# Performance work log

Hardware: AMD Instinct MI355X
Metric: run time of the kernel (lower is better)

The kernel has to match this reference:

```python
import jax, jax.numpy as jnp
import numpy as np

EPS = 1e-12  # matches torch F.normalize default eps

def _l2_normalize(v, axis=-1):
    n = jnp.sqrt(jnp.sum(v * v, axis=axis, keepdims=True))
    return v / jnp.maximum(n, EPS)

def setup_inputs() -> dict:
    key = jax.random.key(0)
    k1, k2, k3 = jax.random.split(key, 3)
    B, S, D_IN, D_OUT, T = 4, 4096, 1024, 1024, 1024
    std = 1.0 / np.sqrt(D_IN)
    return {
        "x": jax.random.normal(k1, (B, S, D_IN), dtype=jnp.float32),
        "key_tokens": jax.random.normal(k2, (T, D_IN), dtype=jnp.float32) * std,
        "value_tokens": jax.random.normal(k3, (T, D_OUT), dtype=jnp.float32) * std,
        "temp": jnp.ones((T, 1), dtype=jnp.float32),
    }

def reference(x, key_tokens, value_tokens, temp):
    # x: [B,S,D_in]; key_tokens: [T,D_in]; value_tokens: [T,D_out]; temp: [T,1]
    x_norm = _l2_normalize(x)                      # [B,S,D_in]
    k_norm = _l2_normalize(key_tokens)             # [T,D_in]
    sim = jnp.einsum('bsd,td->bst', x_norm, k_norm)  # [B,S,T]
    sim = sim * jax.nn.sigmoid(temp).reshape(1, 1, -1)
    # mod_softmax: scale each row to RMS-norm sqrt(T), then exact GELU
    T = sim.shape[-1]
    scale = jnp.sqrt(jnp.float32(T)) / jnp.sqrt(jnp.sum(sim * sim, axis=-1, keepdims=True))
    weights = jax.nn.gelu(sim * scale, approximate=False)  # [B,S,T]
    return jnp.einsum('bst,to->bso', weights, value_tokens)  # [B,S,D_out]
```

## Files before the change

### kernel.cpp

```cpp
#include <hip/hip_runtime.h>
#include <math.h>

typedef __attribute__((ext_vector_type(8))) short short8;
typedef __attribute__((ext_vector_type(4))) float floatx4;

__device__ __forceinline__ float bf2f(unsigned short u) {
    union { unsigned int u; float f; } v;
    v.u = ((unsigned int)u) << 16;
    return v.f;
}

__device__ __forceinline__ unsigned short f2bf(float f) {
    union { float f; unsigned int u; } v;
    v.f = f;
    unsigned int r = v.u + 0x7fffu + ((v.u >> 16) & 1u);
    return (unsigned short)(r >> 16);
}

__device__ __forceinline__ void gload16_lds(const void* g, void* l) {
    __builtin_amdgcn_global_load_lds(
        (const __attribute__((address_space(1))) unsigned int*)g,
        (__attribute__((address_space(3))) unsigned int*)l, 16, 0, 0);
}

__device__ __forceinline__ ushort4 cvt4(float4 v, float fa) {
    ushort4 o;
    o.x = f2bf(v.x * fa); o.y = f2bf(v.y * fa);
    o.z = f2bf(v.z * fa); o.w = f2bf(v.w * fa);
    return o;
}

__global__ __launch_bounds__(256) void prep_kernel(
    const float* __restrict__ x, const float* __restrict__ key,
    const float* __restrict__ temp, const float* __restrict__ val,
    unsigned short* __restrict__ xb, unsigned short* __restrict__ kf,
    unsigned short* __restrict__ VT, float* __restrict__ rowsq,
    int M, int T, int D, int Dout, int nRowBlocks) {
    const int bid = blockIdx.x;
    if (bid < nRowBlocks) {
        const int lane = threadIdx.x & 63;
        const int nWaves = nRowBlocks << 2;
        const int totRows = M + T;
        for (int row = (bid << 2) | (int)(threadIdx.x >> 6); row < totRows;
             row += nWaves) {
            const bool isx = row < M;
            const int r = isx ? row : row - M;
            const float4* s4 =
                (const float4*)(isx ? (x + (size_t)r * D) : (key + (size_t)r * D));
            float4 v0 = s4[lane];
            float4 v1 = s4[lane + 64];
            float4 v2 = s4[lane + 128];
            float4 v3 = s4[lane + 192];
            float s = v0.x * v0.x + v0.y * v0.y + v0.z * v0.z + v0.w * v0.w;
            s += v1.x * v1.x + v1.y * v1.y + v1.z * v1.z + v1.w * v1.w;
            s += v2.x * v2.x + v2.y * v2.y + v2.z * v2.z + v2.w * v2.w;
            s += v3.x * v3.x + v3.y * v3.y + v3.z * v3.z + v3.w * v3.w;
#pragma unroll
            for (int o = 32; o > 0; o >>= 1) s += __shfl_xor(s, o, 64);
            float fa = 1.0f / fmaxf(sqrtf(s), 1e-12f);
            if (isx) {
                if (lane == 0) rowsq[r] = 0.0f;
            } else {
                fa = fa / (1.0f + expf(-temp[r]));
            }
            ushort4* dst =
                (ushort4*)(isx ? (xb + (size_t)r * D) : (kf + (size_t)r * D));
            dst[lane] = cvt4(v0, fa);
            dst[lane + 64] = cvt4(v1, fa);
            dst[lane + 128] = cvt4(v2, fa);
            dst[lane + 192] = cvt4(v3, fa);
        }
    } else {
        __shared__ unsigned short tile[64][65];
        const int idx = bid - nRowBlocks;
        const int nCt = Dout >> 6;
        const int c0 = (idx % nCt) * 64;
        const int r0 = (idx / nCt) * 64;
        const int t = threadIdx.x;
        for (int i = t; i < 4096; i += 256) {
            int rr = i >> 6, cc = i & 63;
            tile[rr][cc] = f2bf(val[(size_t)(r0 + rr) * Dout + c0 + cc]);
        }
        __syncthreads();
        for (int i = t; i < 4096; i += 256) {
            int rr = i >> 6, cc = i & 63;
            VT[(size_t)(c0 + rr) * T + r0 + cc] = tile[cc][rr];
        }
    }
}

template <int MODE>
__global__ __launch_bounds__(256, 2) void gemm_pipe(
    const unsigned short* __restrict__ A, const unsigned short* __restrict__ B,
    void* __restrict__ Cv, float* __restrict__ rowsq, int M, int N, int K) {
    __shared__ __align__(16) char smem[73728];
    const int tid = threadIdx.x;
    const int lane = tid & 63;
    const int w = tid >> 6;
    const int wr = w >> 1;
    const int wc = w & 1;
    const int m0 = blockIdx.x * 256;
    const int n0 = blockIdx.y * 128;
    const int q = lane >> 4;
    const int cl = lane & 15;

    const int srow = lane >> 2;
    const int sch = (lane & 3) ^ ((lane & 32) >> 4);
    const unsigned short* gA = A + (size_t)(m0 + w * 16 + srow) * K + sch * 8;
    const unsigned short* gB = B + (size_t)(n0 + w * 16 + srow) * K + sch * 8;
    const unsigned short* rA0 = gA;
    const unsigned short* rA1 = gA + (size_t)64 * K;
    const unsigned short* rA2 = gA + (size_t)128 * K;
    const unsigned short* rA3 = gA + (size_t)192 * K;
    const unsigned short* rB0 = gB;
    const unsigned short* rB1 = gB + (size_t)64 * K;

    char* stA = smem + w * 1024;
    char* stB = stA + 16384;

    const int LB = ((cl * 64 + q * 16) ^ ((lane & 8) << 2));
    const char* rdA = (const char*)smem + LB + wr * 8192;
    const char* rdB = (const char*)smem + LB + 16384 + wc * 4096;

    floatx4 acc[8][4];
#pragma unroll
    for (int i = 0; i < 8; i++)
#pragma unroll
        for (int j = 0; j < 4; j++) acc[i][j] = (floatx4){0.f, 0.f, 0.f, 0.f};

    short8 af0[4], af1[4], bf0[4], bf1[4];

    gload16_lds(rA0, stA);
    gload16_lds(rA1, stA + 4096);
    gload16_lds(rB0, stB);
    gload16_lds(rA2, stA + 8192);
    gload16_lds(rA3, stA + 12288);
    gload16_lds(rB1, stB + 4096);
    gload16_lds(rA0 + 32, stA + 24576);
    gload16_lds(rA1 + 32, stA + 24576 + 4096);
    gload16_lds(rB0 + 32, stB + 24576);
    gload16_lds(rA2 + 32, stA + 24576 + 8192);
    gload16_lds(rA3 + 32, stA + 24576 + 12288);
    gload16_lds(rB1 + 32, stB + 24576 + 4096);
    asm volatile("s_waitcnt vmcnt(6)" ::: "memory");
    __builtin_amdgcn_s_barrier();
    rA0 += 64; rA1 += 64; rA2 += 64; rA3 += 64; rB0 += 64; rB1 += 64;

#define MFMA4(AFR, BF, RO)                                                   \
    _Pragma("unroll") for (int nt = 0; nt < 4; ++nt)                         \
        acc[RO][nt] = __builtin_amdgcn_mfma_f32_16x16x32_bf16(               \
            AFR, BF[nt], acc[RO][nt], 0, 0, 0);

#define STEP3(AFR, BF, RO)                                                   \
    asm volatile("s_waitcnt lgkmcnt(3)" ::: "memory");                       \
    __builtin_amdgcn_sched_barrier(0);                                       \
    MFMA4(AFR, BF, RO)
#define STEP2(AFR, BF, RO)                                                   \
    asm volatile("s_waitcnt lgkmcnt(2)" ::: "memory");                       \
    __builtin_amdgcn_sched_barrier(0);                                       \
    MFMA4(AFR, BF, RO)
#define STEP1(AFR, BF, RO)                                                   \
    asm volatile("s_waitcnt lgkmcnt(1)" ::: "memory");                       \
    __builtin_amdgcn_sched_barrier(0);                                       \
    MFMA4(AFR, BF, RO)
#define STEP0(AFR, BF, RO)                                                   \
    asm volatile("s_waitcnt lgkmcnt(0)" ::: "memory");                       \
    __builtin_amdgcn_sched_barrier(0);                                       \
    MFMA4(AFR, BF, RO)

#define READS_P0(SLOT, BF)                                                   \
    BF[0] = *(const short8*)(rdB + SLOT * 24576);                            \
    BF[1] = *(const short8*)(rdB + SLOT * 24576 + 1024);                     \
    BF[2] = *(const short8*)(rdB + SLOT * 24576 + 2048);                     \
    BF[3] = *(const short8*)(rdB + SLOT * 24576 + 3072);                     \
    __builtin_amdgcn_sched_barrier(0);                                       \
    af0[0] = *(const short8*)(rdA + SLOT * 24576);                           \
    __builtin_amdgcn_sched_barrier(0);                                       \
    af0[1] = *(const short8*)(rdA + SLOT * 24576 + 1024);                    \
    __builtin_amdgcn_sched_barrier(0);                                       \
    af0[2] = *(const short8*)(rdA + SLOT * 24576 + 2048);                    \
    __builtin_amdgcn_sched_barrier(0);                                       \
    af0[3] = *(const short8*)(rdA + SLOT * 24576 + 3072);                    \
    __builtin_amdgcn_sched_barrier(0);

#define READS_P1(SLOT)                                                       \
    af1[0] = *(const short8*)(rdA + SLOT * 24576 + 4096);                    \
    __builtin_amdgcn_sched_barrier(0);                                       \
    af1[1] = *(const short8*)(rdA + SLOT * 24576 + 5120);                    \
    __builtin_amdgcn_sched_barrier(0);                                       \
    af1[2] = *(const short8*)(rdA + SLOT * 24576 + 6144);                    \
    __builtin_amdgcn_sched_barrier(0);                                       \
    af1[3] = *(const short8*)(rdA + SLOT * 24576 + 7168);                    \
    __builtin_amdgcn_sched_barrier(0);

#define TILE(SLOT, SSLOT, BF, KOFF)                                          \
    {                                                                        \
        READS_P0(SLOT, BF)                                                   \
        gload16_lds(rA0 + KOFF, stA + SSLOT * 24576);                        \
        gload16_lds(rA1 + KOFF, stA + SSLOT * 24576 + 4096);                 \
        gload16_lds(rB0 + KOFF, stB + SSLOT * 24576);                        \
        __builtin_amdgcn_s_barrier();                                        \
        __builtin_amdgcn_s_setprio(1);                                       \
        STEP3(af0[0], BF, 0)                                                 \
        STEP2(af0[1], BF, 1)                                                 \
        STEP1(af0[2], BF, 2)                                                 \
        STEP0(af0[3], BF, 3)                                                 \
        __builtin_amdgcn_s_setprio(0);                                       \
        __builtin_amdgcn_s_barrier();                                        \
        READS_P1(SLOT)                                                       \
        gload16_lds(rA2 + KOFF, stA + SSLOT * 24576 + 8192);                 \
        gload16_lds(rA3 + KOFF, stA + SSLOT * 24576 + 12288);                \
        gload16_lds(rB1 + KOFF, stB + SSLOT * 24576 + 4096);                 \
        asm volatile("s_waitcnt vmcnt(6)" ::: "memory");                     \
        __builtin_amdgcn_s_barrier();                                        \
        __builtin_amdgcn_s_setprio(1);                                       \
        STEP3(af1[0], BF, 4)                                                 \
        STEP2(af1[1], BF, 5)                                                 \
        STEP1(af1[2], BF, 6)                                                 \
        STEP0(af1[3], BF, 7)                                                 \
        __builtin_amdgcn_s_setprio(0);                                       \
        __builtin_amdgcn_s_barrier();                                        \
    }

#define TILE_TAIL(SLOT, BF, DRAIN)                                           \
    {                                                                        \
        READS_P0(SLOT, BF)                                                   \
        __builtin_amdgcn_s_barrier();                                        \
        __builtin_amdgcn_s_setprio(1);                                       \
        STEP3(af0[0], BF, 0)                                                 \
        STEP2(af0[1], BF, 1)                                                 \
        STEP1(af0[2], BF, 2)                                                 \
        STEP0(af0[3], BF, 3)                                                 \
        __builtin_amdgcn_s_setprio(0);                                       \
        __builtin_amdgcn_s_barrier();                                        \
        READS_P1(SLOT)                                                       \
        if (DRAIN) asm volatile("s_waitcnt vmcnt(0)" ::: "memory");          \
        __builtin_amdgcn_s_barrier();                                        \
        __builtin_amdgcn_s_setprio(1);                                       \
        STEP3(af1[0], BF, 4)                                                 \
        STEP2(af1[1], BF, 5)                                                 \
        STEP1(af1[2], BF, 6)                                                 \
        STEP0(af1[3], BF, 7)                                                 \
        __builtin_amdgcn_s_setprio(0);                                       \
        __builtin_amdgcn_s_barrier();                                        \
    }

    for (int g = 0; g < 5; ++g) {
        TILE(0, 2, bf0, 0)
        TILE(1, 0, bf1, 32)
        TILE(2, 1, bf0, 64)
        TILE(0, 2, bf1, 96)
        TILE(1, 0, bf0, 128)
        TILE(2, 1, bf1, 160)
        rA0 += 192; rA1 += 192; rA2 += 192; rA3 += 192;
        rB0 += 192; rB1 += 192;
    }
    TILE_TAIL(0, bf0, 1)
    TILE_TAIL(1, bf1, 0)

#undef TILE
#undef TILE_TAIL
#undef READS_P0
#undef READS_P1
#undef STEP3
#undef STEP2
#undef STEP1
#undef STEP0
#undef MFMA4

#pragma unroll
    for (int mt = 0; mt < 8; ++mt) {
#pragma unroll
        for (int r = 0; r < 4; ++r) {
            const int m = m0 + wr * 128 + mt * 16 + q * 4 + r;
            if (MODE == 0) {
                unsigned short* C = (unsigned short*)Cv;
                float ssq = 0.f;
#pragma unroll
                for (int nt = 0; nt < 4; ++nt) {
                    float v = acc[mt][nt][r];
                    ssq += v * v;
                    C[(size_t)m * N + n0 + wc * 64 + nt * 16 + cl] = f2bf(v);
                }
#pragma unroll
                for (int o = 1; o < 16; o <<= 1) ssq += __shfl_xor(ssq, o, 64);
                if (cl == 0) atomicAdd(&rowsq[m], ssq);
            } else {
                float* C = (float*)Cv;
#pragma unroll
                for (int nt = 0; nt < 4; ++nt)
                    C[(size_t)m * N + n0 + wc * 64 + nt * 16 + cl] =
                        acc[mt][nt][r];
            }
        }
    }
}

__global__ __launch_bounds__(256) void gelu_kernel(unsigned short* __restrict__ sim,
                                                   const float* __restrict__ rowsq,
                                                   int nVec, int t8shift,
                                                   float sqrtT) {
    const int stride = gridDim.x * blockDim.x;
    const float kk = 0.70710678118654752f;
    for (int i = blockIdx.x * blockDim.x + threadIdx.x; i < nVec; i += stride) {
        short8 v = *(const short8*)(sim + (size_t)i * 8);
        const int row = i >> t8shift;
        const float scale = sqrtT / fmaxf(sqrtf(rowsq[row]), 1e-30f);
        short8 o;
#pragma unroll
        for (int j = 0; j < 8; j++) {
            float z = bf2f((unsigned short)v[j]) * scale;
            o[j] = (short)f2bf(0.5f * z * (1.0f + erff(z * kk)));
        }
        *(short8*)(sim + (size_t)i * 8) = o;
    }
}

extern "C" void kernel_launch(void* const* d_in, const int* in_sizes, int n_in,
                              void* d_out, int out_size, void* d_ws, size_t ws_size,
                              hipStream_t stream) {
    const float* x    = (const float*)d_in[0];
    const float* key  = (const float*)d_in[1];
    const float* val  = (const float*)d_in[2];
    const float* temp = (const float*)d_in[3];
    float* out = (float*)d_out;

    const int T = in_sizes[3];
    const int D = in_sizes[1] / T;
    const int Dout = in_sizes[2] / T;
    const int M = in_sizes[0] / D;

    char* ws = (char*)d_ws;
    size_t off = 0;
    unsigned short* xb  = (unsigned short*)(ws + off); off += (size_t)M * D * 2;
    unsigned short* sim = (unsigned short*)(ws + off); off += (size_t)M * T * 2;
    unsigned short* kf  = (unsigned short*)(ws + off); off += (size_t)T * D * 2;
    unsigned short* VT  = (unsigned short*)(ws + off); off += (size_t)Dout * T * 2;
    float* rowsq = (float*)(ws + off); off += (size_t)M * 4;
    (void)ws_size; (void)n_in; (void)out_size;

    const int nTrTiles = (T >> 6) * (Dout >> 6);
    const int nRowBlocks = 1024;
    prep_kernel<<<nRowBlocks + nTrTiles, 256, 0, stream>>>(
        x, key, temp, val, xb, kf, VT, rowsq, M, T, D, Dout, nRowBlocks);
    gemm_pipe<0><<<dim3(M / 256, T / 128), 256, 0, stream>>>(xb, kf, sim, rowsq,
                                                             M, T, D);
    int t8shift = 0;
    {
        int t8 = T >> 3;
        while ((1 << t8shift) < t8) t8shift++;
    }
    gelu_kernel<<<2048, 256, 0, stream>>>(sim, rowsq, M * (T >> 3), t8shift,
                                          sqrtf((float)T));
    gemm_pipe<1><<<dim3(M / 256, Dout / 128), 256, 0, stream>>>(sim, VT, out,
                                                                nullptr, M, Dout, T);
}
```

Before: 219.3 us.

## Fuse GELU normalization into first GEMM epilogue via per-row-block spin barrier

Removes the separate GELU kernel. The first GEMM now holds its accumulators, adds row sum-of-squares atomically, then waits on a per-row-block counter until every column block has contributed, and applies scale and exact GELU before writing bf16. This drops a full read and write pass over the similarity matrix and one launch. The spin barrier assumes all 8 column-blocks of a row-block are co-resident (grid 64x8=512 blocks at 2 per CU, which fits 256 CUs), so it risks deadlock or stalls if they are not, and blocks that finish early sit idle.

```diff
diff --git a/kernel.cpp b/kernel.cpp
--- a/kernel.cpp
+++ b/kernel.cpp
@@ -35,8 +35,10 @@
     const float* __restrict__ temp, const float* __restrict__ val,
     unsigned short* __restrict__ xb, unsigned short* __restrict__ kf,
     unsigned short* __restrict__ VT, float* __restrict__ rowsq,
+    int* __restrict__ cnt,
     int M, int T, int D, int Dout, int nRowBlocks) {
     const int bid = blockIdx.x;
+    if (bid == 0 && threadIdx.x < 64) cnt[threadIdx.x] = 0;
     if (bid < nRowBlocks) {
         const int lane = threadIdx.x & 63;
         const int nWaves = nRowBlocks << 2;
@@ -92,7 +94,8 @@
 template <int MODE>
 __global__ __launch_bounds__(256, 2) void gemm_pipe(
     const unsigned short* __restrict__ A, const unsigned short* __restrict__ B,
-    void* __restrict__ Cv, float* __restrict__ rowsq, int M, int N, int K) {
+    void* __restrict__ Cv, float* __restrict__ rowsq, int* __restrict__ cnt,
+    int M, int N, int K) {
     __shared__ __align__(16) char smem[73728];
     const int tid = threadIdx.x;
     const int lane = tid & 63;
@@ -268,51 +271,63 @@
 #undef STEP0
 #undef MFMA4
 
-#pragma unroll
-    for (int mt = 0; mt < 8; ++mt) {
-#pragma unroll
-        for (int r = 0; r < 4; ++r) {
-            const int m = m0 + wr * 128 + mt * 16 + q * 4 + r;
-            if (MODE == 0) {
-                unsigned short* C = (unsigned short*)Cv;
+    if (MODE == 0) {
+#pragma unroll
+        for (int mt = 0; mt < 8; ++mt) {
+#pragma unroll
+            for (int r = 0; r < 4; ++r) {
                 float ssq = 0.f;
 #pragma unroll
                 for (int nt = 0; nt < 4; ++nt) {
                     float v = acc[mt][nt][r];
                     ssq += v * v;
-                    C[(size_t)m * N + n0 + wc * 64 + nt * 16 + cl] = f2bf(v);
                 }
 #pragma unroll
                 for (int o = 1; o < 16; o <<= 1) ssq += __shfl_xor(ssq, o, 64);
-                if (cl == 0) atomicAdd(&rowsq[m], ssq);
-            } else {
-                float* C = (float*)Cv;
+                if (cl == 0)
+                    atomicAdd(&rowsq[m0 + wr * 128 + mt * 16 + q * 4 + r], ssq);
+            }
+        }
+        __syncthreads();
+        const int NB = (int)gridDim.y;
+        if (tid == 0) {
+            __threadfence();
+            atomicAdd(&cnt[blockIdx.x], 1);
+            while (atomicAdd(&cnt[blockIdx.x], 0) < NB)
+                __builtin_amdgcn_s_sleep(16);
+        }
+        __syncthreads();
+        __threadfence();
+        const float sqrtN = sqrtf((float)N);
+        const float kk = 0.70710678118654752f;
+        unsigned short* C = (unsigned short*)Cv;
+#pragma unroll
+        for (int mt = 0; mt < 8; ++mt) {
+#pragma unroll
+            for (int r = 0; r < 4; ++r) {
+                const int m = m0 + wr * 128 + mt * 16 + q * 4 + r;
+                const float scale = sqrtN / fmaxf(sqrtf(rowsq[m]), 1e-30f);
+#pragma unroll
+                for (int nt = 0; nt < 4; ++nt) {
+                    float z = acc[mt][nt][r] * scale;
+                    float gz = 0.5f * z * (1.0f + erff(z * kk));
+                    C[(size_t)m * N + n0 + wc * 64 + nt * 16 + cl] = f2bf(gz);
+                }
+            }
+        }
+    } else {
+        float* C = (float*)Cv;
+#pragma unroll
+        for (int mt = 0; mt < 8; ++mt) {
+#pragma unroll
+            for (int r = 0; r < 4; ++r) {
+                const int m = m0 + wr * 128 + mt * 16 + q * 4 + r;
 #pragma unroll
                 for (int nt = 0; nt < 4; ++nt)
                     C[(size_t)m * N + n0 + wc * 64 + nt * 16 + cl] =
                         acc[mt][nt][r];
             }
         }
-    }
-}
-
-__global__ __launch_bounds__(256) void gelu_kernel(unsigned short* __restrict__ sim,
-                                                   const float* __restrict__ rowsq,
-                                                   int nVec, int t8shift,
-                                                   float sqrtT) {
-    const int stride = gridDim.x * blockDim.x;
-    const float kk = 0.70710678118654752f;
-    for (int i = blockIdx.x * blockDim.x + threadIdx.x; i < nVec; i += stride) {
-        short8 v = *(const short8*)(sim + (size_t)i * 8);
-        const int row = i >> t8shift;
-        const float scale = sqrtT / fmaxf(sqrtf(rowsq[row]), 1e-30f);
-        short8 o;
-#pragma unroll
-        for (int j = 0; j < 8; j++) {
-            float z = bf2f((unsigned short)v[j]) * scale;
-            o[j] = (short)f2bf(0.5f * z * (1.0f + erff(z * kk)));
-        }
-        *(short8*)(sim + (size_t)i * 8) = o;
     }
 }
 
@@ -337,21 +352,15 @@
     unsigned short* kf  = (unsigned short*)(ws + off); off += (size_t)T * D * 2;
     unsigned short* VT  = (unsigned short*)(ws + off); off += (size_t)Dout * T * 2;
     float* rowsq = (float*)(ws + off); off += (size_t)M * 4;
+    int* cnt = (int*)(ws + off); off += 256 * 4;
     (void)ws_size; (void)n_in; (void)out_size;
 
     const int nTrTiles = (T >> 6) * (Dout >> 6);
     const int nRowBlocks = 1024;
     prep_kernel<<<nRowBlocks + nTrTiles, 256, 0, stream>>>(
-        x, key, temp, val, xb, kf, VT, rowsq, M, T, D, Dout, nRowBlocks);
+        x, key, temp, val, xb, kf, VT, rowsq, cnt, M, T, D, Dout, nRowBlocks);
     gemm_pipe<0><<<dim3(M / 256, T / 128), 256, 0, stream>>>(xb, kf, sim, rowsq,
-                                                             M, T, D);
-    int t8shift = 0;
-    {
-        int t8 = T >> 3;
-        while ((1 << t8shift) < t8) t8shift++;
-    }
-    gelu_kernel<<<2048, 256, 0, stream>>>(sim, rowsq, M * (T >> 3), t8shift,
-                                          sqrtf((float)T));
-    gemm_pipe<1><<<dim3(M / 256, Dout / 128), 256, 0, stream>>>(sim, VT, out,
-                                                                nullptr, M, Dout, T);
-}
+                                                             cnt, M, T, D);
+    gemm_pipe<1><<<dim3(M / 256, Dout / 128), 256, 0, stream>>>(
+        sim, VT, out, nullptr, nullptr, M, Dout, T);
+}
```

Result: slower. 281.6 us (+28.4%).
